# Performance work log

Measured on AMD Instinct MI355X. Metric: run time of the kernel, lower is better.

## Reference

```python
import jax, jax.numpy as jnp
import numpy as np

BS, G, L, D = 64, 64, 100, 64


def setup_inputs() -> dict:
    key = jax.random.key(0)
    ks = jax.random.split(key, 12)
    s = 1.0 / np.sqrt(D)
    return {
        "seqs": jax.random.normal(ks[0], (BS, G, L, D), dtype=jnp.float32),
        "lens": jax.random.randint(ks[1], (BS, G, 1), 1, L + 1, dtype=jnp.int32),
        "W1": jax.random.normal(ks[2], (D, D), dtype=jnp.float32) * s,
        "W2": jax.random.normal(ks[3], (D, D), dtype=jnp.float32) * s,
        "W3": jax.random.normal(ks[4], (D, D), dtype=jnp.float32) * s,
        "b": jnp.zeros((D,), dtype=jnp.float32),
        "p": jax.random.normal(ks[5], (D,), dtype=jnp.float32) * s,
        "Wq": jax.random.normal(ks[6], (D, 2 * D), dtype=jnp.float32) * s,
        "Wl_0": jax.random.normal(ks[7], (2 * D, 2 * D), dtype=jnp.float32) * s,
        "bl_0": jnp.zeros((2 * D,), dtype=jnp.float32),
        "Wl_1": jax.random.normal(ks[8], (2 * D, 2 * D), dtype=jnp.float32) * s,
        "bl_1": jnp.zeros((2 * D,), dtype=jnp.float32),
    }


def reference(seqs, lens, W1, W2, W3, b, p, Wq, Wl_0, bl_0, Wl_1, bl_1):
    # seqs: [bs, g, L, d]; lens: [bs, g, 1]
    V_last = jnp.einsum('bgd,de->bge', seqs[:, :, -1, :], W1)[:, :, None, :]
    V_seq = jnp.einsum('bgld,de->bgle', seqs, W2)
    avg = jnp.sum(seqs, axis=-2) / lens.astype(jnp.float32)  # [bs, g, d]
    V_avg = jnp.einsum('bgd,de->bge', avg, W3)[:, :, None, :]
    emb = jnp.einsum('bgld,d->bgl', V_last + V_seq + V_avg + b, p)  # [bs, g, L]
    attn = jax.nn.softmax(emb, axis=-1)
    weighted = jnp.einsum('bgl,bgld->bgd', attn, seqs)  # attention-weighted pooling
    h0 = weighted @ Wq  # [bs, g, 2d]
    h = jax.nn.relu(h0 @ Wl_0 + bl_0)
    h = jax.nn.relu(h @ Wl_1 + bl_1)
    return h0 + h  # residual
```

## Files before the change

### kernel.cpp

```cpp
#include <hip/hip_runtime.h>
#include <cstddef>

#define BSZ 64
#define GG  64
#define LL  100
#define DD  64
#define NG  4

__global__ void precompute_kernel(const float* __restrict__ W1,
                                  const float* __restrict__ W2,
                                  const float* __restrict__ W3,
                                  const float* __restrict__ b,
                                  const float* __restrict__ p,
                                  float* __restrict__ q) {
    int d = threadIdx.x;
    float s1 = 0.f, s2 = 0.f, s3 = 0.f;
    for (int e = 0; e < DD; ++e) {
        float pe = p[e];
        s1 += W1[d * DD + e] * pe;
        s2 += W2[d * DD + e] * pe;
        s3 += W3[d * DD + e] * pe;
    }
    q[d] = s1; q[DD + d] = s2; q[2 * DD + d] = s3;
    float t = b[d] * p[d];
    #pragma unroll
    for (int off = 32; off > 0; off >>= 1) t += __shfl_down(t, off);
    if (d == 0) q[3 * DD] = t;
}

__global__ __launch_bounds__(256) void seq_encoder_kernel(
    const float* __restrict__ seqs, const int* __restrict__ lens,
    const float* __restrict__ q,
    const float* __restrict__ Wq,  const float* __restrict__ Wl0,
    const float* __restrict__ bl0, const float* __restrict__ Wl1,
    const float* __restrict__ bl1, float* __restrict__ out) {
    __shared__ float s_attn[LL];
    __shared__ float s_part[4][DD];
    __shared__ float s_last[DD];
    __shared__ float s_w[NG][DD];
    __shared__ float s_h0[NG][2 * DD];
    __shared__ float s_h1[NG][2 * DD];

    const int tid = threadIdx.x;
    const int r = tid >> 6;
    const int d = tid & 63;
    const float q1d = q[d], q2d = q[DD + d], q3d = q[2 * DD + d], bp = q[3 * DD];

    for (int i = 0; i < NG; ++i) {
        const int gi = blockIdx.x * NG + i;
        const float* S = seqs + (size_t)gi * (LL * DD);
        float xr[25];
        float csum = 0.f;
        #pragma unroll
        for (int k = 0; k < 25; ++k) {
            int l = r + 4 * k;
            float x = S[l * DD + d];
            xr[k] = x;
            csum += x;
        }
        #pragma unroll
        for (int k = 0; k < 25; ++k) {
            float t = xr[k] * q2d;
            #pragma unroll
            for (int off = 32; off > 0; off >>= 1) t += __shfl_down(t, off);
            if (d == 0) s_attn[r + 4 * k] = t;
        }
        s_part[r][d] = csum;
        if (r == 3) s_last[d] = xr[24];
        __syncthreads();

        if (r == 0) {
            float tot = s_part[0][d] + s_part[1][d] + s_part[2][d] + s_part[3][d];
            float avg = tot / (float)lens[gi];
            float t = s_last[d] * q1d + avg * q3d;
            #pragma unroll
            for (int off = 32; off > 0; off >>= 1) t += __shfl_xor(t, off);
            float c = t + bp;
            float e0 = s_attn[d] + c;
            float e1 = (d < LL - 64) ? (s_attn[64 + d] + c) : -1e30f;
            float m = fmaxf(e0, e1);
            #pragma unroll
            for (int off = 32; off > 0; off >>= 1) m = fmaxf(m, __shfl_xor(m, off));
            float x0 = __expf(e0 - m);
            float x1 = (d < LL - 64) ? __expf(e1 - m) : 0.f;
            float s = x0 + x1;
            #pragma unroll
            for (int off = 32; off > 0; off >>= 1) s += __shfl_xor(s, off);
            float inv = 1.f / s;
            s_attn[d] = x0 * inv;
            if (d < LL - 64) s_attn[64 + d] = x1 * inv;
        }
        __syncthreads();

        float wp = 0.f;
        #pragma unroll
        for (int k = 0; k < 25; ++k) wp += s_attn[r + 4 * k] * xr[k];
        s_part[r][d] = wp;
        __syncthreads();
        if (r == 0)
            s_w[i][d] = s_part[0][d] + s_part[1][d] + s_part[2][d] + s_part[3][d];
        __syncthreads();
    }

    const int jt = tid & 127;
    const int i0 = (tid >> 7) * 2;
    float h0a = 0.f, h0b = 0.f;
    for (int dd2 = 0; dd2 < DD; ++dd2) {
        float w = Wq[dd2 * (2 * DD) + jt];
        h0a += s_w[i0][dd2] * w;
        h0b += s_w[i0 + 1][dd2] * w;
    }
    s_h0[i0][jt] = h0a;
    s_h0[i0 + 1][jt] = h0b;
    __syncthreads();

    float a1 = bl0[jt], b1 = bl0[jt];
    for (int k = 0; k < 2 * DD; ++k) {
        float w = Wl0[k * (2 * DD) + jt];
        a1 += s_h0[i0][k] * w;
        b1 += s_h0[i0 + 1][k] * w;
    }
    a1 = fmaxf(a1, 0.f); b1 = fmaxf(b1, 0.f);
    s_h1[i0][jt] = a1;
    s_h1[i0 + 1][jt] = b1;
    __syncthreads();

    float a2 = bl1[jt], b2 = bl1[jt];
    for (int k = 0; k < 2 * DD; ++k) {
        float w = Wl1[k * (2 * DD) + jt];
        a2 += s_h1[i0][k] * w;
        b2 += s_h1[i0 + 1][k] * w;
    }
    a2 = fmaxf(a2, 0.f); b2 = fmaxf(b2, 0.f);

    const size_t gbase = (size_t)blockIdx.x * NG;
    out[(gbase + i0) * (2 * DD) + jt]     = h0a + a2;
    out[(gbase + i0 + 1) * (2 * DD) + jt] = h0b + b2;
}

extern "C" void kernel_launch(void* const* d_in, const int* in_sizes, int n_in,
                              void* d_out, int out_size, void* d_ws, size_t ws_size,
                              hipStream_t stream) {
    const float* seqs = (const float*)d_in[0];
    const int*   lens = (const int*)d_in[1];
    const float* W1   = (const float*)d_in[2];
    const float* W2   = (const float*)d_in[3];
    const float* W3   = (const float*)d_in[4];
    const float* b    = (const float*)d_in[5];
    const float* p    = (const float*)d_in[6];
    const float* Wq   = (const float*)d_in[7];
    const float* Wl0  = (const float*)d_in[8];
    const float* bl0  = (const float*)d_in[9];
    const float* Wl1  = (const float*)d_in[10];
    const float* bl1  = (const float*)d_in[11];
    float* out = (float*)d_out;
    float* q   = (float*)d_ws;

    precompute_kernel<<<1, 64, 0, stream>>>(W1, W2, W3, b, p, q);
    seq_encoder_kernel<<<(BSZ * GG) / NG, 256, 0, stream>>>(
        seqs, lens, q, Wq, Wl0, bl0, Wl1, bl1, out);
}
```

Measured before the change: 197.7 us.

## Fuse precompute, drop softmax-invariant terms, use online softmax per wave

Removes the separate precompute kernel and computes W2·p inside each block. It drops the V_last, V_avg and bias terms because they add a per-group constant to every logit, which softmax ignores, so lens, W1, W3 and b are no longer read. Each wave now handles one group with float4 loads, DPP row reductions and an online softmax in a single streaming pass, replacing the per-group loop with several block barriers. Every block recomputes q2, which is a small redundant cost.

After: 263.9 us. 33.5% more time.

```diff
diff --git a/kernel.cpp b/kernel.cpp
--- a/kernel.cpp
+++ b/kernel.cpp
@@ -1,152 +1,138 @@
 #include <hip/hip_runtime.h>
 #include <cstddef>
 
-#define BSZ 64
-#define GG  64
-#define LL  100
-#define DD  64
-#define NG  4
+#define LL 100
+#define DD 64
+#define NG 4
 
-__global__ void precompute_kernel(const float* __restrict__ W1,
-                                  const float* __restrict__ W2,
-                                  const float* __restrict__ W3,
-                                  const float* __restrict__ b,
-                                  const float* __restrict__ p,
-                                  float* __restrict__ q) {
-    int d = threadIdx.x;
-    float s1 = 0.f, s2 = 0.f, s3 = 0.f;
-    for (int e = 0; e < DD; ++e) {
-        float pe = p[e];
-        s1 += W1[d * DD + e] * pe;
-        s2 += W2[d * DD + e] * pe;
-        s3 += W3[d * DD + e] * pe;
-    }
-    q[d] = s1; q[DD + d] = s2; q[2 * DD + d] = s3;
-    float t = b[d] * p[d];
-    #pragma unroll
-    for (int off = 32; off > 0; off >>= 1) t += __shfl_down(t, off);
-    if (d == 0) q[3 * DD] = t;
+template<int CTRL>
+__device__ __forceinline__ float dpp_add(float x) {
+    int s = __builtin_amdgcn_update_dpp(0, __float_as_int(x), CTRL, 0xF, 0xF, true);
+    return x + __int_as_float(s);
 }
 
-__global__ __launch_bounds__(256) void seq_encoder_kernel(
-    const float* __restrict__ seqs, const int* __restrict__ lens,
-    const float* __restrict__ q,
+__device__ __forceinline__ float readlane_f(float v, int lane) {
+    return __int_as_float(__builtin_amdgcn_readlane(__float_as_int(v), lane));
+}
+
+__global__ __launch_bounds__(256, 4) void seq_encoder_fused(
+    const float* __restrict__ seqs,
+    const float* __restrict__ W2,  const float* __restrict__ p,
     const float* __restrict__ Wq,  const float* __restrict__ Wl0,
     const float* __restrict__ bl0, const float* __restrict__ Wl1,
-    const float* __restrict__ bl1, float* __restrict__ out) {
-    __shared__ float s_attn[LL];
-    __shared__ float s_part[4][DD];
-    __shared__ float s_last[DD];
-    __shared__ float s_w[NG][DD];
+    const float* __restrict__ bl1, float* __restrict__ out)
+{
+    __shared__ __align__(16) float s_q2[DD];
+    __shared__ __align__(16) float s_w[NG][DD];
     __shared__ float s_h0[NG][2 * DD];
     __shared__ float s_h1[NG][2 * DD];
 
     const int tid = threadIdx.x;
     const int r = tid >> 6;
-    const int d = tid & 63;
-    const float q1d = q[d], q2d = q[DD + d], q3d = q[2 * DD + d], bp = q[3 * DD];
+    const int lane = tid & 63;
 
-    for (int i = 0; i < NG; ++i) {
-        const int gi = blockIdx.x * NG + i;
-        const float* S = seqs + (size_t)gi * (LL * DD);
-        float xr[25];
-        float csum = 0.f;
+    {
+        const int row = tid >> 2, part = tid & 3;
+        const float* wrow = W2 + row * DD + part * 16;
+        const float* pp = p + part * 16;
+        float s = 0.f;
         #pragma unroll
-        for (int k = 0; k < 25; ++k) {
-            int l = r + 4 * k;
-            float x = S[l * DD + d];
-            xr[k] = x;
-            csum += x;
-        }
-        #pragma unroll
-        for (int k = 0; k < 25; ++k) {
-            float t = xr[k] * q2d;
-            #pragma unroll
-            for (int off = 32; off > 0; off >>= 1) t += __shfl_down(t, off);
-            if (d == 0) s_attn[r + 4 * k] = t;
-        }
-        s_part[r][d] = csum;
-        if (r == 3) s_last[d] = xr[24];
-        __syncthreads();
+        for (int e = 0; e < 16; ++e) s += wrow[e] * pp[e];
+        s += __shfl_down(s, 2);
+        s += __shfl_down(s, 1);
+        if (part == 0) s_q2[row] = s;
+    }
+    __syncthreads();
 
-        if (r == 0) {
-            float tot = s_part[0][d] + s_part[1][d] + s_part[2][d] + s_part[3][d];
-            float avg = tot / (float)lens[gi];
-            float t = s_last[d] * q1d + avg * q3d;
-            #pragma unroll
-            for (int off = 32; off > 0; off >>= 1) t += __shfl_xor(t, off);
-            float c = t + bp;
-            float e0 = s_attn[d] + c;
-            float e1 = (d < LL - 64) ? (s_attn[64 + d] + c) : -1e30f;
-            float m = fmaxf(e0, e1);
-            #pragma unroll
-            for (int off = 32; off > 0; off >>= 1) m = fmaxf(m, __shfl_xor(m, off));
-            float x0 = __expf(e0 - m);
-            float x1 = (d < LL - 64) ? __expf(e1 - m) : 0.f;
-            float s = x0 + x1;
-            #pragma unroll
-            for (int off = 32; off > 0; off >>= 1) s += __shfl_xor(s, off);
-            float inv = 1.f / s;
-            s_attn[d] = x0 * inv;
-            if (d < LL - 64) s_attn[64 + d] = x1 * inv;
-        }
-        __syncthreads();
+    const int rg = lane >> 4;
+    const int cb = lane & 15;
+    const float4 q2v = *(const float4*)&s_q2[cb * 4];
 
-        float wp = 0.f;
-        #pragma unroll
-        for (int k = 0; k < 25; ++k) wp += s_attn[r + 4 * k] * xr[k];
-        s_part[r][d] = wp;
-        __syncthreads();
-        if (r == 0)
-            s_w[i][d] = s_part[0][d] + s_part[1][d] + s_part[2][d] + s_part[3][d];
-        __syncthreads();
+    const int gi = blockIdx.x * NG + r;
+    const float4* Sp = (const float4*)(seqs + (size_t)gi * (LL * DD)) + (rg * 16 + cb);
+
+    float m = -1e30f, z = 0.f;
+    float wx = 0.f, wy = 0.f, wz = 0.f, ww = 0.f;
+
+    #pragma unroll
+    for (int it = 0; it < LL / 4; ++it) {
+        float4 x = Sp[it * 64];
+        float t = x.x * q2v.x + x.y * q2v.y + x.z * q2v.z + x.w * q2v.w;
+        t = dpp_add<0x111>(t);
+        t = dpp_add<0x112>(t);
+        t = dpp_add<0x114>(t);
+        t = dpp_add<0x118>(t);
+        float t0 = readlane_f(t, 15);
+        float t1 = readlane_f(t, 31);
+        float t2 = readlane_f(t, 47);
+        float t3 = readlane_f(t, 63);
+        float mn = fmaxf(m, fmaxf(fmaxf(t0, t1), fmaxf(t2, t3)));
+        float sc = __expf(m - mn);
+        float e0 = __expf(t0 - mn), e1 = __expf(t1 - mn);
+        float e2 = __expf(t2 - mn), e3 = __expf(t3 - mn);
+        z = z * sc + (e0 + e1 + e2 + e3);
+        float er = (rg == 0) ? e0 : (rg == 1) ? e1 : (rg == 2) ? e2 : e3;
+        wx = wx * sc + er * x.x;
+        wy = wy * sc + er * x.y;
+        wz = wz * sc + er * x.z;
+        ww = ww * sc + er * x.w;
+        m = mn;
     }
+
+    wx += __shfl_xor(wx, 16); wx += __shfl_xor(wx, 32);
+    wy += __shfl_xor(wy, 16); wy += __shfl_xor(wy, 32);
+    wz += __shfl_xor(wz, 16); wz += __shfl_xor(wz, 32);
+    ww += __shfl_xor(ww, 16); ww += __shfl_xor(ww, 32);
+
+    const float invz = 1.f / z;
+    if (rg == 0) {
+        float4 o;
+        o.x = wx * invz; o.y = wy * invz; o.z = wz * invz; o.w = ww * invz;
+        *(float4*)&s_w[r][cb * 4] = o;
+    }
+    __syncthreads();
 
     const int jt = tid & 127;
     const int i0 = (tid >> 7) * 2;
     float h0a = 0.f, h0b = 0.f;
-    for (int dd2 = 0; dd2 < DD; ++dd2) {
-        float w = Wq[dd2 * (2 * DD) + jt];
-        h0a += s_w[i0][dd2] * w;
-        h0b += s_w[i0 + 1][dd2] * w;
+    for (int k = 0; k < DD; ++k) {
+        float wv = Wq[k * (2 * DD) + jt];
+        h0a += s_w[i0][k] * wv;
+        h0b += s_w[i0 + 1][k] * wv;
     }
     s_h0[i0][jt] = h0a;
     s_h0[i0 + 1][jt] = h0b;
     __syncthreads();
 
-    float a1 = bl0[jt], b1 = bl0[jt];
+    float a1m = bl0[jt], b1m = bl0[jt];
     for (int k = 0; k < 2 * DD; ++k) {
-        float w = Wl0[k * (2 * DD) + jt];
-        a1 += s_h0[i0][k] * w;
-        b1 += s_h0[i0 + 1][k] * w;
+        float wv = Wl0[k * (2 * DD) + jt];
+        a1m += s_h0[i0][k] * wv;
+        b1m += s_h0[i0 + 1][k] * wv;
     }
-    a1 = fmaxf(a1, 0.f); b1 = fmaxf(b1, 0.f);
-    s_h1[i0][jt] = a1;
-    s_h1[i0 + 1][jt] = b1;
+    a1m = fmaxf(a1m, 0.f); b1m = fmaxf(b1m, 0.f);
+    s_h1[i0][jt] = a1m;
+    s_h1[i0 + 1][jt] = b1m;
     __syncthreads();
 
-    float a2 = bl1[jt], b2 = bl1[jt];
+    float a2m = bl1[jt], b2m = bl1[jt];
     for (int k = 0; k < 2 * DD; ++k) {
-        float w = Wl1[k * (2 * DD) + jt];
-        a2 += s_h1[i0][k] * w;
-        b2 += s_h1[i0 + 1][k] * w;
+        float wv = Wl1[k * (2 * DD) + jt];
+        a2m += s_h1[i0][k] * wv;
+        b2m += s_h1[i0 + 1][k] * wv;
     }
-    a2 = fmaxf(a2, 0.f); b2 = fmaxf(b2, 0.f);
+    a2m = fmaxf(a2m, 0.f); b2m = fmaxf(b2m, 0.f);
 
     const size_t gbase = (size_t)blockIdx.x * NG;
-    out[(gbase + i0) * (2 * DD) + jt]     = h0a + a2;
-    out[(gbase + i0 + 1) * (2 * DD) + jt] = h0b + b2;
+    out[(gbase + i0) * (2 * DD) + jt]     = h0a + a2m;
+    out[(gbase + i0 + 1) * (2 * DD) + jt] = h0b + b2m;
 }
 
 extern "C" void kernel_launch(void* const* d_in, const int* in_sizes, int n_in,
                               void* d_out, int out_size, void* d_ws, size_t ws_size,
                               hipStream_t stream) {
     const float* seqs = (const float*)d_in[0];
-    const int*   lens = (const int*)d_in[1];
-    const float* W1   = (const float*)d_in[2];
     const float* W2   = (const float*)d_in[3];
-    const float* W3   = (const float*)d_in[4];
-    const float* b    = (const float*)d_in[5];
     const float* p    = (const float*)d_in[6];
     const float* Wq   = (const float*)d_in[7];
     const float* Wl0  = (const float*)d_in[8];
@@ -154,9 +140,8 @@
     const float* Wl1  = (const float*)d_in[10];
     const float* bl1  = (const float*)d_in[11];
     float* out = (float*)d_out;
-    float* q   = (float*)d_ws;
 
-    precompute_kernel<<<1, 64, 0, stream>>>(W1, W2, W3, b, p, q);
-    seq_encoder_kernel<<<(BSZ * GG) / NG, 256, 0, stream>>>(
-        seqs, lens, q, Wq, Wl0, bl0, Wl1, bl1, out);
+    const int n_groups = 64 * 64;
+    seq_encoder_fused<<<n_groups / NG, 256, 0, stream>>>(
+        seqs, W2, p, Wq, Wl0, bl0, Wl1, bl1, out);
 }
```
